# Kernel tuning notes

Hardware: AMD Instinct MI355X
Metric: run time of the kernel (lower is better)

## Reference

```python
import jax, jax.numpy as jnp
import numpy as np

BN_EPS = 1e-5


def setup_inputs() -> dict:
    key = jax.random.key(0)
    k1, k2, k3, k4 = jax.random.split(key, 4)
    B, S, D = 64, 4096, 256
    x_h = jax.random.normal(k1, (B, 1, D), dtype=jnp.float32)
    x_hpre = jax.random.normal(k2, (B, S, D), dtype=jnp.float32)
    W1 = jax.random.normal(k3, (D, D), dtype=jnp.float32) * (1.0 / np.sqrt(D))
    W2 = jax.random.normal(k4, (D, 1), dtype=jnp.float32)
    gamma = jnp.ones((S,), dtype=jnp.float32)
    beta = jnp.zeros((S,), dtype=jnp.float32)
    running_mean = jnp.zeros((S,), dtype=jnp.float32)
    running_var = jnp.ones((S,), dtype=jnp.float32)
    return {"x_h": x_h, "x_hpre": x_hpre, "W1": W1, "W2": W2,
            "gamma": gamma, "beta": beta,
            "running_mean": running_mean, "running_var": running_var}


def reference(x_h, x_hpre, W1, W2, gamma, beta, running_mean, running_var):
    # fc1 (no bias): [B,S,D] @ W1^T
    h = jnp.einsum('bsd,ed->bse', x_hpre, W1)
    # BatchNorm1d over channel dim S (eval mode, running stats)
    inv = jax.lax.rsqrt(running_var + BN_EPS)                # [S]
    h = (h - running_mean[None, :, None]) * inv[None, :, None]
    h = h * gamma[None, :, None] + beta[None, :, None]
    h = jnp.tanh(h)
    # Dropout1d is identity in eval mode.
    # a_t = h @ x_h^T : [B,S,D] @ [B,D,1] -> [B,S,1]
    a_t = jnp.einsum('bsd,bd->bs', h, x_h[:, 0, :])          # [B,S]
    a_s = jax.nn.softmax(a_t, axis=1)                        # softmax over seq dim
    # fc2: Linear(1, D): ATT[b,s,d] = a_s[b,s] * W2[d,0]
    # loop-sum over seq: out[b,d] = sum_s ATT[b,s,d] * x_hpre[b,s,d]
    out = jnp.einsum('bs,d,bsd->bd', a_s, W2[:, 0], x_hpre)  # [B,D]
    return out[:, None, :]                                   # [B,1,D]
```

## Files before the change

kernel.cpp:

```cpp
#include <hip/hip_runtime.h>

#define BN_EPS 1e-5f

typedef _Float16 half8 __attribute__((ext_vector_type(8)));
typedef float f32x4 __attribute__((ext_vector_type(4)));

__device__ __forceinline__ float tanh_fast(float x){
  float e = __expf(2.0f * x);
  return 1.0f - 2.0f / (e + 1.0f);
}

__global__ __launch_bounds__(256) void k_prep(const float* __restrict__ W1,
    const float* __restrict__ gamma, const float* __restrict__ beta,
    const float* __restrict__ rmean, const float* __restrict__ rvar,
    _Float16* __restrict__ Bp2, float* __restrict__ bns, float* __restrict__ bnb){
  int i = blockIdx.x * 256 + threadIdx.x;
  int j  = i & 7;
  int l  = (i >> 3) & 63;
  int c  = (i >> 9) & 15;
  int q  = (i >> 13) & 7;
  int lr = l & 15, kg = l >> 4;
  int e  = c * 16 + lr;
  int d  = q * 32 + kg * 8 + j;
  Bp2[i] = (_Float16)W1[e * 256 + d];
  if (i < 4096){
    float sc = gamma[i] * rsqrtf(rvar[i] + BN_EPS);
    bns[i] = sc;
    bnb[i] = beta[i] - rmean[i] * sc;
  }
}

__global__ __launch_bounds__(256) void k_fused(const float* __restrict__ xh,
    const float* __restrict__ xhpre, const _Float16* __restrict__ Bp,
    const float* __restrict__ bns, const float* __restrict__ bnb,
    float* __restrict__ Pbuf, float2* __restrict__ mz){
  constexpr int S = 4096, Dd = 256;
  const int bid = blockIdx.x;
  const int b  = bid >> 6;
  const int s0 = (bid & 63) * 64;
  const int tid = threadIdx.x;
  const int lane = tid & 63;
  const int w = tid >> 6;
  const int kg = lane >> 4;
  const int lr = lane & 15;

  __shared__ _Float16 A[64 * 256];
  __shared__ float bnsc[64], bnsh[64];
  __shared__ float red[4][64];
  __shared__ f32x4 red4[4][64];
  __shared__ float wrow[64];
  char* Ab = (char*)A;

  if (tid < 64){ bnsc[tid] = bns[s0 + tid]; bnsh[tid] = bnb[s0 + tid]; }

  float xhv[4];
  #pragma unroll
  for (int nt = 0; nt < 4; ++nt) xhv[nt] = xh[b * 256 + w * 64 + nt * 16 + lr];

  const float* Abase = xhpre + ((size_t)b * S + s0) * Dd;

  {
    int row = w * 16 + kg;
    float4 v = *reinterpret_cast<const float4*>(Abase + (size_t)row * Dd + lr * 4);
    union { _Float16 h[4]; uint2 u; } pk;
    pk.h[0]=(_Float16)v.x; pk.h[1]=(_Float16)v.y; pk.h[2]=(_Float16)v.z; pk.h[3]=(_Float16)v.w;
    int byte = (row * 512 + lr * 8) ^ ((row & 7) << 4);
    *reinterpret_cast<uint2*>(Ab + byte) = pk.u;
  }
  #pragma unroll
  for (int i = 1; i < 4; ++i){
    int row = w * 16 + i * 4 + kg;
    float4 v = *reinterpret_cast<const float4*>(Abase + (size_t)row * Dd + lr * 4);
    union { _Float16 h[4]; uint2 u; } pk;
    pk.h[0]=(_Float16)v.x; pk.h[1]=(_Float16)v.y; pk.h[2]=(_Float16)v.z; pk.h[3]=(_Float16)v.w;
    int byte = (row * 512 + lr * 8) ^ ((row & 7) << 4);
    *reinterpret_cast<uint2*>(Ab + byte) = pk.u;
  }
  __syncthreads();

  f32x4 acc[4][4] = {};

  #pragma unroll
  for (int k0 = 0; k0 < 4; ++k0){
    float4 nv[4];
    if (k0 < 3){
      #pragma unroll
      for (int i = 0; i < 4; ++i){
        int row = w * 16 + i * 4 + kg;
        nv[i] = *reinterpret_cast<const float4*>(Abase + (size_t)row * Dd + (k0 + 1) * 64 + lr * 4);
      }
    }

    #pragma unroll
    for (int kk = 0; kk < 2; ++kk){
      const int q = k0 * 2 + kk;
      half8 afr[4], bfr[4];
      #pragma unroll
      for (int nt = 0; nt < 4; ++nt)
        bfr[nt] = *reinterpret_cast<const half8*>(Bp + ((size_t)((q * 16 + w * 4 + nt) * 64 + lane)) * 8);
      #pragma unroll
      for (int mt = 0; mt < 4; ++mt){
        int row = mt * 16 + lr;
        int byte = (row * 512 + k0 * 128 + kk * 64 + kg * 16) ^ ((row & 7) << 4);
        afr[mt] = *reinterpret_cast<const half8*>(Ab + byte);
      }
      #pragma unroll
      for (int mt = 0; mt < 4; ++mt)
        #pragma unroll
        for (int nt = 0; nt < 4; ++nt)
          acc[mt][nt] = __builtin_amdgcn_mfma_f32_16x16x32_f16(afr[mt], bfr[nt], acc[mt][nt], 0, 0, 0);
    }

    if (k0 < 3){
      #pragma unroll
      for (int i = 0; i < 4; ++i){
        int row = w * 16 + i * 4 + kg;
        union { _Float16 h[4]; uint2 u; } pk;
        pk.h[0]=(_Float16)nv[i].x; pk.h[1]=(_Float16)nv[i].y;
        pk.h[2]=(_Float16)nv[i].z; pk.h[3]=(_Float16)nv[i].w;
        int byte = (row * 512 + (k0 + 1) * 128 + lr * 8) ^ ((row & 7) << 4);
        *reinterpret_cast<uint2*>(Ab + byte) = pk.u;
      }
    }
    __syncthreads();
  }

  #pragma unroll
  for (int mt = 0; mt < 4; ++mt){
    #pragma unroll
    for (int r = 0; r < 4; ++r){
      int row = mt * 16 + kg * 4 + r;
      float sc = bnsc[row], sh = bnsh[row];
      float sum = 0.f;
      #pragma unroll
      for (int nt = 0; nt < 4; ++nt){
        float hv = fmaf(acc[mt][nt][r], sc, sh);
        sum = fmaf(tanh_fast(hv), xhv[nt], sum);
      }
      sum += __shfl_xor(sum, 1);
      sum += __shfl_xor(sum, 2);
      sum += __shfl_xor(sum, 4);
      sum += __shfl_xor(sum, 8);
      if (lr == 0) red[w][row] = sum;
    }
  }
  __syncthreads();

  if (w == 0){
    float v = red[0][lane] + red[1][lane] + red[2][lane] + red[3][lane];
    float m_c = v;
    #pragma unroll
    for (int o = 1; o < 64; o <<= 1) m_c = fmaxf(m_c, __shfl_xor(m_c, o));
    float wv = __expf(v - m_c);
    wrow[lane] = wv;
    float z_c = wv;
    #pragma unroll
    for (int o = 1; o < 64; o <<= 1) z_c += __shfl_xor(z_c, o);
    if (lane == 0) mz[bid] = make_float2(m_c, z_c);
  }
  __syncthreads();

  f32x4 pacc = {0.f, 0.f, 0.f, 0.f};
  #pragma unroll
  for (int r = 0; r < 16; ++r){
    int row = w * 16 + r;
    float wgt = wrow[row];
    int byte = (row * 512 + lane * 8) ^ ((row & 7) << 4);
    union { _Float16 h[4]; uint2 u; } pk;
    pk.u = *reinterpret_cast<const uint2*>(Ab + byte);
    pacc[0] = fmaf(wgt, (float)pk.h[0], pacc[0]);
    pacc[1] = fmaf(wgt, (float)pk.h[1], pacc[1]);
    pacc[2] = fmaf(wgt, (float)pk.h[2], pacc[2]);
    pacc[3] = fmaf(wgt, (float)pk.h[3], pacc[3]);
  }
  red4[w][lane] = pacc;
  __syncthreads();
  if (tid < 64){
    f32x4 r = red4[0][tid] + red4[1][tid] + red4[2][tid] + red4[3][tid];
    *reinterpret_cast<f32x4*>(Pbuf + (size_t)bid * 256 + tid * 4) = r;
  }
}

__global__ __launch_bounds__(256) void k_combine(const float* __restrict__ Pbuf,
    const float2* __restrict__ mz, const float* __restrict__ W2, float* __restrict__ out){
  int b = blockIdx.x, d = threadIdx.x;
  __shared__ float2 smz[64];
  if (d < 64) smz[d] = mz[b * 64 + d];
  __syncthreads();
  float M = smz[0].x;
  #pragma unroll
  for (int c = 1; c < 64; ++c) M = fmaxf(M, smz[c].x);
  float Z = 0.f, acc = 0.f;
  #pragma unroll 8
  for (int c = 0; c < 64; ++c){
    float e = __expf(smz[c].x - M);
    Z += smz[c].y * e;
    acc = fmaf(e, Pbuf[(size_t)(b * 64 + c) * 256 + d], acc);
  }
  out[b * 256 + d] = acc * W2[d] / Z;
}

extern "C" void kernel_launch(void* const* d_in, const int* in_sizes, int n_in,
                              void* d_out, int out_size, void* d_ws, size_t ws_size,
                              hipStream_t stream){
  const float* x_h    = (const float*)d_in[0];
  const float* x_hpre = (const float*)d_in[1];
  const float* W1     = (const float*)d_in[2];
  const float* W2     = (const float*)d_in[3];
  const float* gamma  = (const float*)d_in[4];
  const float* beta   = (const float*)d_in[5];
  const float* rmean  = (const float*)d_in[6];
  const float* rvar   = (const float*)d_in[7];
  float* out = (float*)d_out;

  char* ws = (char*)d_ws;
  _Float16* Bp = (_Float16*)(ws);
  float* bns   = (float*)(ws + 131072);
  float* bnb   = (float*)(ws + 147456);
  float* Pbuf  = (float*)(ws + 163840);
  float2* mzb  = (float2*)(ws + 4358144);

  hipLaunchKernelGGL(k_prep,    dim3(256),  dim3(256), 0, stream, W1, gamma, beta, rmean, rvar, Bp, bns, bnb);
  hipLaunchKernelGGL(k_fused,   dim3(4096), dim3(256), 0, stream, x_h, x_hpre, Bp, bns, bnb, Pbuf, mzb);
  hipLaunchKernelGGL(k_combine, dim3(64),   dim3(256), 0, stream, Pbuf, mzb, W2, out);
}
```

Baseline: 97.76 us.

## Issue all x_hpre chunk loads up front and split GEMM into two barrier phases

Instead of loading one 64-column chunk per k-step with a barrier each step, all four chunks of the x_hpre tile are issued early into registers. The first two are converted and written to LDS before the first half of the MFMA loop, and the last two during it. This cuts barriers from four to two and keeps more global loads in flight to hide HBM latency. A launch bound of 4 blocks per SM is also requested, which caps registers while 64 floats of staging now stay live, so spills or lower effective occupancy are a risk.

```diff
diff --git a/kernel.cpp b/kernel.cpp
--- a/kernel.cpp
+++ b/kernel.cpp
@@ -30,7 +30,7 @@
   }
 }
 
-__global__ __launch_bounds__(256) void k_fused(const float* __restrict__ xh,
+__global__ __launch_bounds__(256, 4) void k_fused(const float* __restrict__ xh,
     const float* __restrict__ xhpre, const _Float16* __restrict__ Bp,
     const float* __restrict__ bns, const float* __restrict__ bnb,
     float* __restrict__ Pbuf, float2* __restrict__ mz){
@@ -59,71 +59,74 @@
 
   const float* Abase = xhpre + ((size_t)b * S + s0) * Dd;
 
-  {
-    int row = w * 16 + kg;
-    float4 v = *reinterpret_cast<const float4*>(Abase + (size_t)row * Dd + lr * 4);
-    union { _Float16 h[4]; uint2 u; } pk;
-    pk.h[0]=(_Float16)v.x; pk.h[1]=(_Float16)v.y; pk.h[2]=(_Float16)v.z; pk.h[3]=(_Float16)v.w;
-    int byte = (row * 512 + lr * 8) ^ ((row & 7) << 4);
-    *reinterpret_cast<uint2*>(Ab + byte) = pk.u;
-  }
-  #pragma unroll
-  for (int i = 1; i < 4; ++i){
-    int row = w * 16 + i * 4 + kg;
-    float4 v = *reinterpret_cast<const float4*>(Abase + (size_t)row * Dd + lr * 4);
-    union { _Float16 h[4]; uint2 u; } pk;
-    pk.h[0]=(_Float16)v.x; pk.h[1]=(_Float16)v.y; pk.h[2]=(_Float16)v.z; pk.h[3]=(_Float16)v.w;
-    int byte = (row * 512 + lr * 8) ^ ((row & 7) << 4);
-    *reinterpret_cast<uint2*>(Ab + byte) = pk.u;
-  }
-  __syncthreads();
+#define ISSUE(buf, c) \
+  _Pragma("unroll") \
+  for (int i = 0; i < 4; ++i){ \
+    int row = w * 16 + i * 4 + kg; \
+    buf[i] = *reinterpret_cast<const float4*>(Abase + (size_t)row * Dd + (c) * 64 + lr * 4); \
+  }
+#define CVTW(buf, c) \
+  _Pragma("unroll") \
+  for (int i = 0; i < 4; ++i){ \
+    int row = w * 16 + i * 4 + kg; \
+    union { _Float16 h[4]; uint2 u; } pk; \
+    pk.h[0]=(_Float16)buf[i].x; pk.h[1]=(_Float16)buf[i].y; \
+    pk.h[2]=(_Float16)buf[i].z; pk.h[3]=(_Float16)buf[i].w; \
+    int byte = (row * 512 + (c) * 128 + lr * 8) ^ ((row & 7) << 4); \
+    *reinterpret_cast<uint2*>(Ab + byte) = pk.u; \
+  }
+
+  float4 bufA[4], bufB[4], bufC[4], bufD[4];
+  ISSUE(bufA, 0); ISSUE(bufB, 1);
+  CVTW(bufA, 0);  ISSUE(bufC, 2);
+  CVTW(bufB, 1);  ISSUE(bufD, 3);
+  asm volatile("s_waitcnt lgkmcnt(0)" ::: "memory");
+  __builtin_amdgcn_s_barrier();
 
   f32x4 acc[4][4] = {};
 
   #pragma unroll
-  for (int k0 = 0; k0 < 4; ++k0){
-    float4 nv[4];
-    if (k0 < 3){
-      #pragma unroll
-      for (int i = 0; i < 4; ++i){
-        int row = w * 16 + i * 4 + kg;
-        nv[i] = *reinterpret_cast<const float4*>(Abase + (size_t)row * Dd + (k0 + 1) * 64 + lr * 4);
-      }
+  for (int q = 0; q < 4; ++q){
+    half8 afr[4], bfr[4];
+    #pragma unroll
+    for (int nt = 0; nt < 4; ++nt)
+      bfr[nt] = *reinterpret_cast<const half8*>(Bp + ((size_t)((q * 16 + w * 4 + nt) * 64 + lane)) * 8);
+    #pragma unroll
+    for (int mt = 0; mt < 4; ++mt){
+      int row = mt * 16 + lr;
+      int byte = (row * 512 + q * 64 + kg * 16) ^ ((row & 7) << 4);
+      afr[mt] = *reinterpret_cast<const half8*>(Ab + byte);
     }
-
-    #pragma unroll
-    for (int kk = 0; kk < 2; ++kk){
-      const int q = k0 * 2 + kk;
-      half8 afr[4], bfr[4];
+    #pragma unroll
+    for (int mt = 0; mt < 4; ++mt)
       #pragma unroll
       for (int nt = 0; nt < 4; ++nt)
-        bfr[nt] = *reinterpret_cast<const half8*>(Bp + ((size_t)((q * 16 + w * 4 + nt) * 64 + lane)) * 8);
+        acc[mt][nt] = __builtin_amdgcn_mfma_f32_16x16x32_f16(afr[mt], bfr[nt], acc[mt][nt], 0, 0, 0);
+  }
+
+  CVTW(bufC, 2); CVTW(bufD, 3);
+  __syncthreads();
+
+  #pragma unroll
+  for (int q = 4; q < 8; ++q){
+    half8 afr[4], bfr[4];
+    #pragma unroll
+    for (int nt = 0; nt < 4; ++nt)
+      bfr[nt] = *reinterpret_cast<const half8*>(Bp + ((size_t)((q * 16 + w * 4 + nt) * 64 + lane)) * 8);
+    #pragma unroll
+    for (int mt = 0; mt < 4; ++mt){
+      int row = mt * 16 + lr;
+      int byte = (row * 512 + q * 64 + kg * 16) ^ ((row & 7) << 4);
+      afr[mt] = *reinterpret_cast<const half8*>(Ab + byte);
+    }
+    #pragma unroll
+    for (int mt = 0; mt < 4; ++mt)
       #pragma unroll
-      for (int mt = 0; mt < 4; ++mt){
-        int row = mt * 16 + lr;
-        int byte = (row * 512 + k0 * 128 + kk * 64 + kg * 16) ^ ((row & 7) << 4);
-        afr[mt] = *reinterpret_cast<const half8*>(Ab + byte);
-      }
-      #pragma unroll
-      for (int mt = 0; mt < 4; ++mt)
-        #pragma unroll
-        for (int nt = 0; nt < 4; ++nt)
-          acc[mt][nt] = __builtin_amdgcn_mfma_f32_16x16x32_f16(afr[mt], bfr[nt], acc[mt][nt], 0, 0, 0);
-    }
-
-    if (k0 < 3){
-      #pragma unroll
-      for (int i = 0; i < 4; ++i){
-        int row = w * 16 + i * 4 + kg;
-        union { _Float16 h[4]; uint2 u; } pk;
-        pk.h[0]=(_Float16)nv[i].x; pk.h[1]=(_Float16)nv[i].y;
-        pk.h[2]=(_Float16)nv[i].z; pk.h[3]=(_Float16)nv[i].w;
-        int byte = (row * 512 + (k0 + 1) * 128 + lr * 8) ^ ((row & 7) << 4);
-        *reinterpret_cast<uint2*>(Ab + byte) = pk.u;
-      }
-    }
-    __syncthreads();
-  }
+      for (int nt = 0; nt < 4; ++nt)
+        acc[mt][nt] = __builtin_amdgcn_mfma_f32_16x16x32_f16(afr[mt], bfr[nt], acc[mt][nt], 0, 0, 0);
+  }
+#undef ISSUE
+#undef CVTW
 
   #pragma unroll
   for (int mt = 0; mt < 4; ++mt){
```

Result: slower. 166.3 us (+70.2%).
